# Kernel optimization log

Measured on AMD Instinct MI355X. Metric: run time of the kernel, lower is better.

## Reference

```python
import jax, jax.numpy as jnp
import numpy as np

B, L, D = 2, 1024, 768
NL = 8            # n_layers
DI = 2 * D        # d_inner (expand=2)
NS = 16           # d_state
DR = D // 16      # dt_rank = 48
KC = 4            # d_conv
EPS = 1e-5


def setup_inputs() -> dict:
    key = jax.random.key(0)
    ks = jax.random.split(key, 12)
    s = 0.02
    inp = {
        "x":        jax.random.normal(ks[0], (B, L, D), jnp.float32),
        "ln_w":     jnp.ones((NL, D), jnp.float32),
        "ln_b":     jnp.zeros((NL, D), jnp.float32),
        "in_proj":  jax.random.normal(ks[1], (NL, 2 * DI, D), jnp.float32) * s,
        "conv_w":   jax.random.normal(ks[2], (NL, DI, KC), jnp.float32) * 0.1,
        "conv_b":   jnp.zeros((NL, DI), jnp.float32),
        "x_proj":   jax.random.normal(ks[3], (NL, DR + 2 * NS, DI), jnp.float32) * s,
        "dt_w":     jax.random.normal(ks[4], (NL, DI, DR), jnp.float32) * s,
        "dt_b":     jax.random.normal(ks[5], (NL, DI), jnp.float32) * 0.5,
        "A_log":    jnp.broadcast_to(jnp.log(jnp.arange(1, NS + 1, dtype=jnp.float32)), (NL, DI, NS)).copy(),
        "D_skip":   jnp.ones((NL, DI), jnp.float32),
        "out_proj": jax.random.normal(ks[6], (NL, D, DI), jnp.float32) * s,
        "fn_w":     jnp.ones((D,), jnp.float32),
        "fn_b":     jnp.zeros((D,), jnp.float32),
    }
    return inp


def _layernorm(x, w, b):
    mu = x.mean(-1, keepdims=True)
    var = ((x - mu) ** 2).mean(-1, keepdims=True)
    return (x - mu) * jax.lax.rsqrt(var + EPS) * w + b


def _silu(x):
    return x * jax.nn.sigmoid(x)


def _mamba(xn, Wi, cw, cb, Wx, Wdt, bdt, A_log, Dp, Wo):
    # xn: (B, L, D)
    xz = jnp.einsum('bld,ed->ble', xn, Wi)          # (B, L, 2*DI)
    xi, z = jnp.split(xz, 2, axis=-1)               # each (B, L, DI)
    # causal depthwise conv along L
    xc = jax.lax.conv_general_dilated(
        xi.transpose(0, 2, 1), cw[:, None, :], (1,), [(KC - 1, 0)],
        feature_group_count=DI, dimension_numbers=('NCH', 'OIH', 'NCH'))
    xc = _silu(xc.transpose(0, 2, 1) + cb)          # (B, L, DI)
    dbc = jnp.einsum('ble,re->blr', xc, Wx)         # (B, L, DR+2*NS)
    dt = jax.nn.softplus(jnp.einsum('blr,dr->bld', dbc[..., :DR], Wdt) + bdt)  # (B,L,DI)
    Bm = dbc[..., DR:DR + NS]                        # (B, L, NS)
    Cm = dbc[..., DR + NS:]                          # (B, L, NS)
    A = -jnp.exp(A_log)                              # (DI, NS)

    def step(h, inp):
        dt_t, B_t, C_t, x_t = inp                    # (B,DI),(B,NS),(B,NS),(B,DI)
        dA = jnp.exp(dt_t[..., None] * A)            # (B, DI, NS)
        h = dA * h + (dt_t * x_t)[..., None] * B_t[:, None, :]
        y = jnp.einsum('bdn,bn->bd', h, C_t)
        return h, y

    xs = (dt.transpose(1, 0, 2), Bm.transpose(1, 0, 2),
          Cm.transpose(1, 0, 2), xc.transpose(1, 0, 2))
    h0 = jnp.zeros((xn.shape[0], DI, NS), xn.dtype)
    _, ys = jax.lax.scan(step, h0, xs)               # ys: (L, B, DI)
    y = ys.transpose(1, 0, 2) + xc * Dp
    y = y * _silu(z)
    return jnp.einsum('ble,de->bld', y, Wo)          # (B, L, D)


def reference(x, ln_w, ln_b, in_proj, conv_w, conv_b, x_proj, dt_w, dt_b,
              A_log, D_skip, out_proj, fn_w, fn_b):
    params = (ln_w, ln_b, in_proj, conv_w, conv_b, x_proj, dt_w, dt_b,
              A_log, D_skip, out_proj)

    def block(carry, p):
        xcur, res = carry
        lw, lb, Wi, cw, cb, Wx, Wdt, bdt, Al, Dp, Wo = p
        res = xcur + res                 # residual = x + residual
        xn = _layernorm(xcur, lw, lb)    # norm(x) -- note: norms block input, per source
        h = _mamba(xn, Wi, cw, cb, Wx, Wdt, bdt, Al, Dp, Wo)
        return (h, res), None

    res0 = jnp.zeros_like(x)             # residual=None handled as zeros
    (xf, resf), _ = jax.lax.scan(block, (x, res0), params)
    out = _layernorm(xf + resf, fn_w, fn_b)
    return out
```

## Files before the change

kernel.cpp:

```cpp
#include <hip/hip_runtime.h>
#include <math.h>

#define B_ 2
#define L_ 1024
#define D_ 768
#define NL_ 8
#define DI_ 1536
#define NS_ 16
#define DR_ 48
#define KC_ 4
#define EPS_ 1e-5f
#define M_ (B_*L_)
#define NC_ 64
#define T_ 16
#define KS_ 16
#define KCH_ (DI_/KS_)
#define KDT_ 64

typedef short bf16x8 __attribute__((ext_vector_type(8)));
typedef float f32x4  __attribute__((ext_vector_type(4)));

__device__ __forceinline__ unsigned short f2bf(float f) {
    union { float f; unsigned int u; } v; v.f = f;
    unsigned int u = v.u;
    u += 0x7fffu + ((u >> 16) & 1u);
    return (unsigned short)(u >> 16);
}

__device__ __forceinline__ unsigned int pk2(float a, float b) {
    union { float f; unsigned int u; } va, vb;
    va.f = a; vb.f = b;
    unsigned int ua = va.u + (0x7fffu + ((va.u >> 16) & 1u));
    unsigned int ub = vb.u + (0x7fffu + ((vb.u >> 16) & 1u));
    return (ua >> 16) | (ub & 0xffff0000u);
}

__device__ __forceinline__ void gload16(const void* g, void* l) {
    __builtin_amdgcn_global_load_lds(
        (const __attribute__((address_space(1))) void*)g,
        (__attribute__((address_space(3))) void*)l, 16, 0, 0);
}

__device__ __forceinline__ void cvt_blk(const float* __restrict__ s,
                                        unsigned short* __restrict__ d, int tid) {
    #pragma unroll
    for (int r = 0; r < 4; r++) {
        int off = tid * 4 + r * 1024;
        float4 a = *(const float4*)&s[off];
        uint2 o = {pk2(a.x, a.y), pk2(a.z, a.w)};
        *(uint2*)&d[off] = o;
    }
}

__global__ __launch_bounds__(256) void prep_kernel(
    const float* __restrict__ wi, unsigned short* __restrict__ wi_bf,
    const float* __restrict__ wo, unsigned short* __restrict__ wo_bf,
    const float* __restrict__ wx, unsigned short* __restrict__ wx_bf,
    const float* __restrict__ wdt, unsigned short* __restrict__ wdt_bf,
    const float* __restrict__ A_log, float* __restrict__ negA,
    const float* __restrict__ x, float* __restrict__ xcur,
    float* __restrict__ res,
    unsigned short* __restrict__ dbc_bf) {
    const int E0 = NL_ * 2 * DI_ * D_;
    const int E1 = NL_ * D_ * DI_;
    const int E2 = NL_ * 80 * DI_;
    const int E3 = NL_ * DI_ * KDT_;
    const int E4 = NL_ * DI_ * NS_;
    const int E5 = M_ * D_;
    int tid = threadIdx.x;
    int base = blockIdx.x * 4096;
    if (base < E0) { cvt_blk(wi + base, wi_bf + base, tid); return; }
    base -= E0;
    if (base < E1) { cvt_blk(wo + base, wo_bf + base, tid); return; }
    base -= E1;
    if (base < E2) { cvt_blk(wx + base, wx_bf + base, tid); return; }
    base -= E2;
    if (base < E3) {
        #pragma unroll
        for (int r = 0; r < 4; r++) {
            int off = base + tid * 4 + r * 1024;
            int col = off & (KDT_ - 1);
            uint2 o = {0u, 0u};
            if (col < DR_) {
                float4 a = *(const float4*)&wdt[(size_t)(off >> 6) * DR_ + col];
                o = (uint2){pk2(a.x, a.y), pk2(a.z, a.w)};
            }
            *(uint2*)&wdt_bf[off] = o;
        }
        return;
    }
    base -= E3;
    if (base < E4) {
        #pragma unroll
        for (int r = 0; r < 4; r++) {
            int off = base + tid * 4 + r * 1024;
            float4 a = *(const float4*)&A_log[off];
            float4 o = make_float4(-__expf(a.x), -__expf(a.y),
                                   -__expf(a.z), -__expf(a.w));
            *(float4*)&negA[off] = o;
        }
        return;
    }
    base -= E4;
    if (base < E5) {
        float4 z = make_float4(0.f, 0.f, 0.f, 0.f);
        #pragma unroll
        for (int r = 0; r < 4; r++) {
            int off = base + tid * 4 + r * 1024;
            *(float4*)&xcur[off] = *(const float4*)&x[off];
            *(float4*)&res[off] = z;
        }
        return;
    }
    base -= E5;
    {
        #pragma unroll
        for (int r = 0; r < 4; r++) {
            int off = base + tid * 4 + r * 1024;
            *(uint2*)&dbc_bf[off] = (uint2){0u, 0u};
        }
    }
}

__device__ __forceinline__ float block_sum256(float v) {
    __shared__ float sb[4];
    #pragma unroll
    for (int o = 32; o > 0; o >>= 1) v += __shfl_down(v, o);
    if ((threadIdx.x & 63) == 0) sb[threadIdx.x >> 6] = v;
    __syncthreads();
    float r = sb[0] + sb[1] + sb[2] + sb[3];
    __syncthreads();
    return r;
}

__global__ __launch_bounds__(256) void ln_res_kernel(
    const float* __restrict__ xcur, float* __restrict__ res,
    const float* __restrict__ w, const float* __restrict__ b,
    unsigned short* __restrict__ xn) {
    int row = blockIdx.x;
    int t = threadIdx.x;
    size_t base = (size_t)row * D_;
    float v0 = xcur[base + t];
    float v1 = xcur[base + t + 256];
    float v2 = xcur[base + t + 512];
    res[base + t]       += v0;
    res[base + t + 256] += v1;
    res[base + t + 512] += v2;
    float mu = block_sum256(v0 + v1 + v2) * (1.0f / D_);
    float d0 = v0 - mu, d1 = v1 - mu, d2 = v2 - mu;
    float var = block_sum256(d0 * d0 + d1 * d1 + d2 * d2) * (1.0f / D_);
    float rs = rsqrtf(var + EPS_);
    xn[base + t]       = f2bf(d0 * rs * w[t]       + b[t]);
    xn[base + t + 256] = f2bf(d1 * rs * w[t + 256] + b[t + 256]);
    xn[base + t + 512] = f2bf(d2 * rs * w[t + 512] + b[t + 512]);
}

__global__ __launch_bounds__(256) void final_ln_kernel(
    const float* __restrict__ xcur, const float* __restrict__ res,
    const float* __restrict__ w, const float* __restrict__ b,
    float* __restrict__ out) {
    int row = blockIdx.x;
    int t = threadIdx.x;
    size_t base = (size_t)row * D_;
    float v0 = xcur[base + t]       + res[base + t];
    float v1 = xcur[base + t + 256] + res[base + t + 256];
    float v2 = xcur[base + t + 512] + res[base + t + 512];
    float mu = block_sum256(v0 + v1 + v2) * (1.0f / D_);
    float d0 = v0 - mu, d1 = v1 - mu, d2 = v2 - mu;
    float var = block_sum256(d0 * d0 + d1 * d1 + d2 * d2) * (1.0f / D_);
    float rs = rsqrtf(var + EPS_);
    out[base + t]       = d0 * rs * w[t]       + b[t];
    out[base + t + 256] = d1 * rs * w[t + 256] + b[t + 256];
    out[base + t + 512] = d2 * rs * w[t + 512] + b[t + 512];
}

template <int BM, int BN>
__global__ __launch_bounds__(256) void gemm_bf16_t(
    const unsigned short* __restrict__ A,
    const unsigned short* __restrict__ W,
    float* __restrict__ C, int M, int N, int K) {
    constexpr int FM = BM / 32;
    constexpr int FN = BN / 32;
    constexpr int NLD = (BM + BN) / 64;
    __shared__ unsigned short sA[BM * 32];
    __shared__ unsigned short sW[BN * 32];
    int bm = blockIdx.y * BM, bn = blockIdx.x * BN;
    int tid = threadIdx.x;
    int wave = tid >> 6, lane = tid & 63;
    int wrow = (wave & 1) * (BM / 2), wcol = (wave >> 1) * (BN / 2);
    int quad = lane >> 4, r16 = lane & 15;
    f32x4 acc[FM][FN];
    #pragma unroll
    for (int i = 0; i < FM; i++)
        #pragma unroll
        for (int j = 0; j < FN; j++)
            acc[i][j] = (f32x4){0.f, 0.f, 0.f, 0.f};

    for (int k0 = 0; k0 < K; k0 += 32) {
        #pragma unroll
        for (int r = 0; r < NLD; r++) {
            if (r < BM / 64) {
                int j = r * 256 + tid;
                gload16(&A[(size_t)(bm + (j >> 2)) * K + k0 + (j & 3) * 8],
                        &sA[(r * 256 + wave * 64) * 8]);
            } else {
                int j = (r - BM / 64) * 256 + tid;
                gload16(&W[(size_t)(bn + (j >> 2)) * K + k0 + (j & 3) * 8],
                        &sW[((r - BM / 64) * 256 + wave * 64) * 8]);
            }
        }
        __syncthreads();
        bf16x8 af[FM], wf[FN];
        #pragma unroll
        for (int i = 0; i < FM; i++)
            af[i] = *(const bf16x8*)&sA[(wrow + i * 16 + r16) * 32 + quad * 8];
        #pragma unroll
        for (int j = 0; j < FN; j++)
            wf[j] = *(const bf16x8*)&sW[(wcol + j * 16 + r16) * 32 + quad * 8];
        #pragma unroll
        for (int i = 0; i < FM; i++)
            #pragma unroll
            for (int j = 0; j < FN; j++)
                acc[i][j] = __builtin_amdgcn_mfma_f32_16x16x32_bf16(
                    af[i], wf[j], acc[i][j], 0, 0, 0);
        __syncthreads();
    }
    #pragma unroll
    for (int i = 0; i < FM; i++) {
        #pragma unroll
        for (int j = 0; j < FN; j++) {
            int col = bn + wcol + j * 16 + r16;
            #pragma unroll
            for (int reg = 0; reg < 4; reg++) {
                int row = bm + wrow + i * 16 + quad * 4 + reg;
                C[(size_t)row * N + col] = acc[i][j][reg];
            }
        }
    }
}

__global__ __launch_bounds__(256) void dt_gemm_bf16(
    const unsigned short* __restrict__ A,
    const unsigned short* __restrict__ W,
    const float* __restrict__ bias,
    float* __restrict__ dtb) {
    __shared__ unsigned short sA[128 * 32];
    __shared__ unsigned short sW[128 * 32];
    int bm = blockIdx.y * 128, bn = blockIdx.x * 128;
    int tid = threadIdx.x;
    int wave = tid >> 6, lane = tid & 63;
    int wrow = (wave & 1) * 64, wcol = (wave >> 1) * 64;
    int quad = lane >> 4, r16 = lane & 15;
    f32x4 acc[4][4];
    #pragma unroll
    for (int i = 0; i < 4; i++)
        #pragma unroll
        for (int j = 0; j < 4; j++)
            acc[i][j] = (f32x4){0.f, 0.f, 0.f, 0.f};

    #pragma unroll
    for (int k0 = 0; k0 < KDT_; k0 += 32) {
        #pragma unroll
        for (int r = 0; r < 4; r++) {
            if (r < 2) {
                int j = r * 256 + tid;
                gload16(&A[(size_t)(bm + (j >> 2)) * KDT_ + k0 + (j & 3) * 8],
                        &sA[(r * 256 + wave * 64) * 8]);
            } else {
                int j = (r - 2) * 256 + tid;
                gload16(&W[(size_t)(bn + (j >> 2)) * KDT_ + k0 + (j & 3) * 8],
                        &sW[((r - 2) * 256 + wave * 64) * 8]);
            }
        }
        __syncthreads();
        bf16x8 af[4], wf[4];
        #pragma unroll
        for (int i = 0; i < 4; i++)
            af[i] = *(const bf16x8*)&sA[(wrow + i * 16 + r16) * 32 + quad * 8];
        #pragma unroll
        for (int j = 0; j < 4; j++)
            wf[j] = *(const bf16x8*)&sW[(wcol + j * 16 + r16) * 32 + quad * 8];
        #pragma unroll
        for (int i = 0; i < 4; i++)
            #pragma unroll
            for (int j = 0; j < 4; j++)
                acc[i][j] = __builtin_amdgcn_mfma_f32_16x16x32_bf16(
                    af[i], wf[j], acc[i][j], 0, 0, 0);
        __syncthreads();
    }
    #pragma unroll
    for (int i = 0; i < 4; i++) {
        #pragma unroll
        for (int j = 0; j < 4; j++) {
            int col = bn + wcol + j * 16 + r16;
            float bv = bias[col];
            #pragma unroll
            for (int reg = 0; reg < 4; reg++) {
                int row = bm + wrow + i * 16 + quad * 4 + reg;
                float v = acc[i][j][reg] + bv;
                v = (v > 20.f) ? v : log1pf(__expf(v));
                dtb[(size_t)row * DI_ + col] = v;
            }
        }
    }
}

__global__ __launch_bounds__(256) void conv_xproj_kernel(
    const float* __restrict__ xz,
    const float* __restrict__ cw,
    const float* __restrict__ cb,
    const unsigned short* __restrict__ W,
    float* __restrict__ xcf,
    float* __restrict__ Pb) {
    __shared__ float sxz[67 * 96];
    __shared__ unsigned short sxcb[64 * 104];
    __shared__ float scw[96 * 4];
    __shared__ float scb[96];
    unsigned short* sW = (unsigned short*)sxz;

    int ks = blockIdx.x;
    int bm = blockIdx.y * 64;
    int tid = threadIdx.x;
    int b = bm >> 10, t0 = bm & (L_ - 1);
    int dbase = ks * KCH_;

    if (tid < 96) {
        int d = dbase + tid;
        *(float4*)&scw[tid * 4] = *(const float4*)&cw[d * 4];
        scb[tid] = cb[d];
    }
    for (int j = tid; j < 67 * 24; j += 256) {
        int r = j / 24, c4 = (j % 24) * 4;
        int tt = t0 + r - 3;
        float4 v = make_float4(0.f, 0.f, 0.f, 0.f);
        if (tt >= 0)
            v = *(const float4*)&xz[((size_t)(b * L_ + tt)) * (2 * DI_) + dbase + c4];
        *(float4*)&sxz[r * 96 + c4] = v;
    }
    __syncthreads();
    for (int j = tid; j < 64 * 96; j += 256) {
        int r = j / 96, c = j % 96;
        float acc = scb[c];
        #pragma unroll
        for (int k = 0; k < KC_; k++)
            acc = fmaf(scw[c * 4 + k], sxz[(r + k) * 96 + c], acc);
        float v = acc / (1.0f + __expf(-acc));
        xcf[(size_t)(bm + r) * DI_ + dbase + c] = v;
        sxcb[r * 104 + c] = f2bf(v);
    }
    __syncthreads();
    for (int j = tid; j < 80 * 12; j += 256) {
        int row = j / 12, c16 = (j % 12) * 8;
        *(uint4*)&sW[row * 104 + c16] =
            *(const uint4*)&W[(size_t)row * DI_ + dbase + c16];
    }
    __syncthreads();
    int wave = tid >> 6, lane = tid & 63;
    int quad = lane >> 4, r16 = lane & 15;
    f32x4 acc[5];
    #pragma unroll
    for (int j = 0; j < 5; j++) acc[j] = (f32x4){0.f, 0.f, 0.f, 0.f};
    #pragma unroll
    for (int kk = 0; kk < 3; kk++) {
        bf16x8 af = *(const bf16x8*)&sxcb[(wave * 16 + r16) * 104 + kk * 32 + quad * 8];
        #pragma unroll
        for (int j = 0; j < 5; j++) {
            bf16x8 wf = *(const bf16x8*)&sW[(j * 16 + r16) * 104 + kk * 32 + quad * 8];
            acc[j] = __builtin_amdgcn_mfma_f32_16x16x32_bf16(af, wf, acc[j], 0, 0, 0);
        }
    }
    #pragma unroll
    for (int j = 0; j < 5; j++) {
        int col = j * 16 + r16;
        #pragma unroll
        for (int reg = 0; reg < 4; reg++) {
            int row = bm + wave * 16 + quad * 4 + reg;
            Pb[((size_t)ks * M_ + row) * 80 + col] = acc[j][reg];
        }
    }
}

__global__ void xproj_reduce_kernel(const float* __restrict__ Pb,
                                    unsigned short* __restrict__ dbc_bf,
                                    float* __restrict__ bcp) {
    int i = blockIdx.x * 256 + threadIdx.x;
    float s = 0.f;
    #pragma unroll
    for (int ks = 0; ks < KS_; ks++) s += Pb[(size_t)ks * (M_ * 80) + i];
    int m = i / 80, col = i % 80;
    if (col < DR_) {
        dbc_bf[m * KDT_ + col] = f2bf(s);
    } else if (col < DR_ + NS_) {
        bcp[m * 32 + 2 * (col - DR_)] = s;
    } else {
        bcp[m * 32 + 2 * (col - DR_ - NS_) + 1] = s;
    }
}

__global__ __launch_bounds__(256) void scan_ps_kernel(
    const float* __restrict__ dtb,
    const float* __restrict__ xcf,
    const float4* __restrict__ bcp4,
    const float* __restrict__ negA,
    float* __restrict__ Sb,
    float* __restrict__ sdb) {
    const int NDB = DI_ / 256;
    int bx = blockIdx.x;
    int dblk = bx % NDB;
    int c = (bx / NDB) % NC_;
    int b = bx / (NDB * NC_);
    int d = dblk * 256 + threadIdx.x;

    float A[NS_];
    #pragma unroll
    for (int n = 0; n < NS_; n++) A[n] = negA[(size_t)d * NS_ + n];
    float h[NS_];
    #pragma unroll
    for (int n = 0; n < NS_; n++) h[n] = 0.f;
    float sd = 0.f;

    size_t btbase = (size_t)(b * L_ + c * T_);
    const float* pdt = dtb + btbase * DI_ + d;
    const float* pxc = xcf + btbase * DI_ + d;
    const float4* pbc = bcp4 + btbase * 8;

    #pragma unroll
    for (int t = 0; t < T_; t++) {
        float dt = pdt[(size_t)t * DI_];
        float u  = dt * pxc[(size_t)t * DI_];
        sd += dt;
        #pragma unroll
        for (int q = 0; q < 8; q++) {
            float4 v = pbc[t * 8 + q];
            float e0 = __expf(dt * A[2 * q]);
            h[2 * q] = fmaf(e0, h[2 * q], u * v.x);
            float e1 = __expf(dt * A[2 * q + 1]);
            h[2 * q + 1] = fmaf(e1, h[2 * q + 1], u * v.z);
        }
    }

    size_t o = (((size_t)b * NC_ + c) * DI_ + d) * NS_;
    #pragma unroll
    for (int n = 0; n < NS_; n++) Sb[o + n] = h[n];
    sdb[((size_t)b * NC_ + c) * DI_ + d] = sd;
}

__global__ __launch_bounds__(256) void scan_combine_kernel(
    const float* __restrict__ Sb, const float* __restrict__ sdb,
    const float* __restrict__ negA, float* __restrict__ hin) {
    int i = blockIdx.x * 256 + threadIdx.x;
    int b = i / (DI_ * NS_);
    int rem = i % (DI_ * NS_);
    int d = rem >> 4;
    float Aa = negA[rem];
    const size_t str = (size_t)DI_ * NS_;
    size_t o = (size_t)b * NC_ * str + rem;
    size_t osd = (size_t)b * NC_ * DI_ + d;
    float h = 0.f;
    float s = Sb[o], sd = sdb[osd];
    #pragma unroll 4
    for (int c = 0; c < NC_ - 1; c++) {
        float sn = Sb[o + str];
        float sdn = sdb[osd + DI_];
        hin[o] = h;
        h = fmaf(__expf(Aa * sd), h, s);
        s = sn; sd = sdn;
        o += str; osd += DI_;
    }
    hin[o] = h;
}

__global__ __launch_bounds__(256) void scan_out_kernel(
    const float* __restrict__ dtb, const float* __restrict__ xcf,
    const float4* __restrict__ bcp4, const float* __restrict__ negA,
    const float* __restrict__ hin, const float* __restrict__ xz,
    const float* __restrict__ Dp, unsigned short* __restrict__ yg) {
    const int NDB = DI_ / 256;
    int bx = blockIdx.x;
    int dblk = bx % NDB;
    int c = (bx / NDB) % NC_;
    int b = bx / (NDB * NC_);
    int d = dblk * 256 + threadIdx.x;

    float A[NS_];
    #pragma unroll
    for (int n = 0; n < NS_; n++) A[n] = negA[(size_t)d * NS_ + n];
    size_t o = (((size_t)b * NC_ + c) * DI_ + d) * NS_;
    float h[NS_];
    #pragma unroll
    for (int n = 0; n < NS_; n++) h[n] = hin[o + n];
    float dpv = Dp[d];

    size_t btbase = (size_t)(b * L_ + c * T_);
    const float* pdt = dtb + btbase * DI_ + d;
    const float* pxc = xcf + btbase * DI_ + d;
    const float4* pbc = bcp4 + btbase * 8;

    #pragma unroll
    for (int t = 0; t < T_; t++) {
        float dt = pdt[(size_t)t * DI_];
        float xc = pxc[(size_t)t * DI_];
        float u = dt * xc;
        float y = 0.f;
        #pragma unroll
        for (int q = 0; q < 8; q++) {
            float4 v = pbc[t * 8 + q];
            float e0 = __expf(dt * A[2 * q]);
            h[2 * q] = fmaf(e0, h[2 * q], u * v.x);
            y = fmaf(v.y, h[2 * q], y);
            float e1 = __expf(dt * A[2 * q + 1]);
            h[2 * q + 1] = fmaf(e1, h[2 * q + 1], u * v.z);
            y = fmaf(v.w, h[2 * q + 1], y);
        }
        size_t row = btbase + t;
        float zv = xz[row * (2 * DI_) + DI_ + d];
        float yy = y + xc * dpv;
        yy *= zv / (1.0f + __expf(-zv));
        yg[row * DI_ + d] = f2bf(yy);
    }
}

extern "C" void kernel_launch(void* const* d_in, const int* in_sizes, int n_in,
                              void* d_out, int out_size, void* d_ws, size_t ws_size,
                              hipStream_t stream) {
    const float* x        = (const float*)d_in[0];
    const float* ln_w     = (const float*)d_in[1];
    const float* ln_b     = (const float*)d_in[2];
    const float* in_proj  = (const float*)d_in[3];
    const float* conv_w   = (const float*)d_in[4];
    const float* conv_b   = (const float*)d_in[5];
    const float* x_proj   = (const float*)d_in[6];
    const float* dt_w     = (const float*)d_in[7];
    const float* dt_b     = (const float*)d_in[8];
    const float* A_log    = (const float*)d_in[9];
    const float* D_skip   = (const float*)d_in[10];
    const float* out_proj = (const float*)d_in[11];
    const float* fn_w     = (const float*)d_in[12];
    const float* fn_b     = (const float*)d_in[13];
    float* out = (float*)d_out;

    char* p = (char*)d_ws;
    auto alloc = [&](size_t bytes) {
        char* r = p;
        p += (bytes + 255) & ~(size_t)255;
        return (void*)r;
    };
    float* xcur = (float*)alloc((size_t)M_ * D_ * 4);
    float* res  = (float*)alloc((size_t)M_ * D_ * 4);
    unsigned short* xn = (unsigned short*)alloc((size_t)M_ * D_ * 2);
    float* xz   = (float*)alloc((size_t)M_ * 2 * DI_ * 4);
    float* dtb  = (float*)alloc((size_t)M_ * DI_ * 4);
    float* xcf  = (float*)alloc((size_t)M_ * DI_ * 4);
    unsigned short* dbc_bf = (unsigned short*)alloc((size_t)M_ * KDT_ * 2);
    float* bcp  = (float*)alloc((size_t)M_ * 32 * 4);
    unsigned short* yg = (unsigned short*)alloc((size_t)M_ * DI_ * 2);
    float* Sb   = (float*)alloc((size_t)B_ * NC_ * DI_ * NS_ * 4);
    float* sdb  = (float*)alloc((size_t)B_ * NC_ * DI_ * 4);
    float* hin  = (float*)alloc((size_t)B_ * NC_ * DI_ * NS_ * 4);
    float* Pb   = (float*)alloc((size_t)KS_ * M_ * 80 * 4);
    float* negA = (float*)alloc((size_t)NL_ * DI_ * NS_ * 4);
    const size_t n_wi = (size_t)NL_ * 2 * DI_ * D_;
    const size_t n_wo = (size_t)NL_ * D_ * DI_;
    const size_t n_wx = (size_t)NL_ * 80 * DI_;
    const size_t n_wdt = (size_t)NL_ * DI_ * KDT_;
    unsigned short* wi_bf = (unsigned short*)alloc(n_wi * 2);
    unsigned short* wo_bf = (unsigned short*)alloc(n_wo * 2);
    unsigned short* wx_bf = (unsigned short*)alloc(n_wx * 2);
    unsigned short* wdt_bf = (unsigned short*)alloc(n_wdt * 2);

    prep_kernel<<<7808, 256, 0, stream>>>(
        in_proj, wi_bf, out_proj, wo_bf, x_proj, wx_bf,
        dt_w, wdt_bf, A_log, negA, x, xcur, res, dbc_bf);

    for (int l = 0; l < NL_; l++) {
        const float* negA_l = negA + (size_t)l * DI_ * NS_;

        ln_res_kernel<<<M_, 256, 0, stream>>>(
            xcur, res, ln_w + l * D_, ln_b + l * D_, xn);

        gemm_bf16_t<128, 128><<<dim3((2 * DI_) / 128, M_ / 128), 256, 0, stream>>>(
            xn, wi_bf + (size_t)l * 2 * DI_ * D_, xz, M_, 2 * DI_, D_);

        conv_xproj_kernel<<<dim3(KS_, M_ / 64), 256, 0, stream>>>(
            xz, conv_w + l * DI_ * KC_, conv_b + l * DI_,
            wx_bf + (size_t)l * 80 * DI_, xcf, Pb);
        xproj_reduce_kernel<<<(M_ * 80) / 256, 256, 0, stream>>>(Pb, dbc_bf, bcp);

        dt_gemm_bf16<<<dim3(DI_ / 128, M_ / 128), 256, 0, stream>>>(
            dbc_bf, wdt_bf + (size_t)l * DI_ * KDT_, dt_b + l * DI_, dtb);

        scan_ps_kernel<<<B_ * NC_ * (DI_ / 256), 256, 0, stream>>>(
            dtb, xcf, (const float4*)bcp, negA_l, Sb, sdb);
        scan_combine_kernel<<<(B_ * DI_ * NS_) / 256, 256, 0, stream>>>(
            Sb, sdb, negA_l, hin);
        scan_out_kernel<<<B_ * NC_ * (DI_ / 256), 256, 0, stream>>>(
            dtb, xcf, (const float4*)bcp, negA_l, hin, xz,
            D_skip + (size_t)l * DI_, yg);

        gemm_bf16_t<128, 64><<<dim3(D_ / 64, M_ / 128), 256, 0, stream>>>(
            yg, wo_bf + (size_t)l * D_ * DI_, xcur, M_, D_, DI_);
    }

    final_ln_kernel<<<M_, 256, 0, stream>>>(xcur, res, fn_w, fn_b, out);
}
```

Before: 1.408 ms.

## Use one wave per row in layernorms, vectorize prep, retune scan combine

```diff
diff --git a/kernel.cpp b/kernel.cpp
--- a/kernel.cpp
+++ b/kernel.cpp
@@ -43,13 +43,15 @@
 
 __device__ __forceinline__ void cvt_blk(const float* __restrict__ s,
                                         unsigned short* __restrict__ d, int tid) {
-    #pragma unroll
-    for (int r = 0; r < 4; r++) {
-        int off = tid * 4 + r * 1024;
-        float4 a = *(const float4*)&s[off];
-        uint2 o = {pk2(a.x, a.y), pk2(a.z, a.w)};
-        *(uint2*)&d[off] = o;
-    }
+    int o = tid * 4;
+    float4 a0 = *(const float4*)&s[o];
+    float4 a1 = *(const float4*)&s[o + 1024];
+    float4 a2 = *(const float4*)&s[o + 2048];
+    float4 a3 = *(const float4*)&s[o + 3072];
+    *(uint2*)&d[o]        = (uint2){pk2(a0.x, a0.y), pk2(a0.z, a0.w)};
+    *(uint2*)&d[o + 1024] = (uint2){pk2(a1.x, a1.y), pk2(a1.z, a1.w)};
+    *(uint2*)&d[o + 2048] = (uint2){pk2(a2.x, a2.y), pk2(a2.z, a2.w)};
+    *(uint2*)&d[o + 3072] = (uint2){pk2(a3.x, a3.y), pk2(a3.z, a3.w)};
 }
 
 __global__ __launch_bounds__(256) void prep_kernel(
@@ -76,102 +78,161 @@
     if (base < E2) { cvt_blk(wx + base, wx_bf + base, tid); return; }
     base -= E2;
     if (base < E3) {
-        #pragma unroll
-        for (int r = 0; r < 4; r++) {
-            int off = base + tid * 4 + r * 1024;
-            int col = off & (KDT_ - 1);
-            uint2 o = {0u, 0u};
-            if (col < DR_) {
-                float4 a = *(const float4*)&wdt[(size_t)(off >> 6) * DR_ + col];
-                o = (uint2){pk2(a.x, a.y), pk2(a.z, a.w)};
-            }
-            *(uint2*)&wdt_bf[off] = o;
+        int off0 = base + tid * 4;
+        int col = off0 & (KDT_ - 1);
+        if (col < DR_) {
+            float4 a0 = *(const float4*)&wdt[(size_t)((off0) >> 6) * DR_ + col];
+            float4 a1 = *(const float4*)&wdt[(size_t)((off0 + 1024) >> 6) * DR_ + col];
+            float4 a2 = *(const float4*)&wdt[(size_t)((off0 + 2048) >> 6) * DR_ + col];
+            float4 a3 = *(const float4*)&wdt[(size_t)((off0 + 3072) >> 6) * DR_ + col];
+            *(uint2*)&wdt_bf[off0]        = (uint2){pk2(a0.x, a0.y), pk2(a0.z, a0.w)};
+            *(uint2*)&wdt_bf[off0 + 1024] = (uint2){pk2(a1.x, a1.y), pk2(a1.z, a1.w)};
+            *(uint2*)&wdt_bf[off0 + 2048] = (uint2){pk2(a2.x, a2.y), pk2(a2.z, a2.w)};
+            *(uint2*)&wdt_bf[off0 + 3072] = (uint2){pk2(a3.x, a3.y), pk2(a3.z, a3.w)};
+        } else {
+            uint2 z = {0u, 0u};
+            *(uint2*)&wdt_bf[off0] = z;
+            *(uint2*)&wdt_bf[off0 + 1024] = z;
+            *(uint2*)&wdt_bf[off0 + 2048] = z;
+            *(uint2*)&wdt_bf[off0 + 3072] = z;
         }
         return;
     }
     base -= E3;
     if (base < E4) {
-        #pragma unroll
-        for (int r = 0; r < 4; r++) {
-            int off = base + tid * 4 + r * 1024;
-            float4 a = *(const float4*)&A_log[off];
-            float4 o = make_float4(-__expf(a.x), -__expf(a.y),
-                                   -__expf(a.z), -__expf(a.w));
-            *(float4*)&negA[off] = o;
-        }
+        int off0 = base + tid * 4;
+        float4 a0 = *(const float4*)&A_log[off0];
+        float4 a1 = *(const float4*)&A_log[off0 + 1024];
+        float4 a2 = *(const float4*)&A_log[off0 + 2048];
+        float4 a3 = *(const float4*)&A_log[off0 + 3072];
+        *(float4*)&negA[off0] = make_float4(-__expf(a0.x), -__expf(a0.y), -__expf(a0.z), -__expf(a0.w));
+        *(float4*)&negA[off0 + 1024] = make_float4(-__expf(a1.x), -__expf(a1.y), -__expf(a1.z), -__expf(a1.w));
+        *(float4*)&negA[off0 + 2048] = make_float4(-__expf(a2.x), -__expf(a2.y), -__expf(a2.z), -__expf(a2.w));
+        *(float4*)&negA[off0 + 3072] = make_float4(-__expf(a3.x), -__expf(a3.y), -__expf(a3.z), -__expf(a3.w));
         return;
     }
     base -= E4;
     if (base < E5) {
+        int off0 = base + tid * 4;
+        float4 a0 = *(const float4*)&x[off0];
+        float4 a1 = *(const float4*)&x[off0 + 1024];
+        float4 a2 = *(const float4*)&x[off0 + 2048];
+        float4 a3 = *(const float4*)&x[off0 + 3072];
         float4 z = make_float4(0.f, 0.f, 0.f, 0.f);
-        #pragma unroll
-        for (int r = 0; r < 4; r++) {
-            int off = base + tid * 4 + r * 1024;
-            *(float4*)&xcur[off] = *(const float4*)&x[off];
-            *(float4*)&res[off] = z;
-        }
+        *(float4*)&xcur[off0] = a0;        *(float4*)&res[off0] = z;
+        *(float4*)&xcur[off0 + 1024] = a1; *(float4*)&res[off0 + 1024] = z;
+        *(float4*)&xcur[off0 + 2048] = a2; *(float4*)&res[off0 + 2048] = z;
+        *(float4*)&xcur[off0 + 3072] = a3; *(float4*)&res[off0 + 3072] = z;
         return;
     }
     base -= E5;
     {
-        #pragma unroll
-        for (int r = 0; r < 4; r++) {
-            int off = base + tid * 4 + r * 1024;
-            *(uint2*)&dbc_bf[off] = (uint2){0u, 0u};
-        }
-    }
-}
-
-__device__ __forceinline__ float block_sum256(float v) {
-    __shared__ float sb[4];
+        int off0 = base + tid * 4;
+        uint2 z = {0u, 0u};
+        *(uint2*)&dbc_bf[off0] = z;
+        *(uint2*)&dbc_bf[off0 + 1024] = z;
+        *(uint2*)&dbc_bf[off0 + 2048] = z;
+        *(uint2*)&dbc_bf[off0 + 3072] = z;
+    }
+}
+
+__device__ __forceinline__ float wave_sum(float v) {
     #pragma unroll
     for (int o = 32; o > 0; o >>= 1) v += __shfl_down(v, o);
-    if ((threadIdx.x & 63) == 0) sb[threadIdx.x >> 6] = v;
-    __syncthreads();
-    float r = sb[0] + sb[1] + sb[2] + sb[3];
-    __syncthreads();
-    return r;
+    return __shfl(v, 0);
 }
 
 __global__ __launch_bounds__(256) void ln_res_kernel(
     const float* __restrict__ xcur, float* __restrict__ res,
     const float* __restrict__ w, const float* __restrict__ b,
     unsigned short* __restrict__ xn) {
-    int row = blockIdx.x;
-    int t = threadIdx.x;
+    int wave = threadIdx.x >> 6, lane = threadIdx.x & 63;
+    int row = blockIdx.x * 4 + wave;
     size_t base = (size_t)row * D_;
-    float v0 = xcur[base + t];
-    float v1 = xcur[base + t + 256];
-    float v2 = xcur[base + t + 512];
-    res[base + t]       += v0;
-    res[base + t + 256] += v1;
-    res[base + t + 512] += v2;
-    float mu = block_sum256(v0 + v1 + v2) * (1.0f / D_);
-    float d0 = v0 - mu, d1 = v1 - mu, d2 = v2 - mu;
-    float var = block_sum256(d0 * d0 + d1 * d1 + d2 * d2) * (1.0f / D_);
+    int off = lane * 4;
+    float4 v0 = *(const float4*)&xcur[base + off];
+    float4 v1 = *(const float4*)&xcur[base + off + 256];
+    float4 v2 = *(const float4*)&xcur[base + off + 512];
+    float4 r0 = *(const float4*)&res[base + off];
+    float4 r1 = *(const float4*)&res[base + off + 256];
+    float4 r2 = *(const float4*)&res[base + off + 512];
+    r0.x += v0.x; r0.y += v0.y; r0.z += v0.z; r0.w += v0.w;
+    r1.x += v1.x; r1.y += v1.y; r1.z += v1.z; r1.w += v1.w;
+    r2.x += v2.x; r2.y += v2.y; r2.z += v2.z; r2.w += v2.w;
+    *(float4*)&res[base + off]       = r0;
+    *(float4*)&res[base + off + 256] = r1;
+    *(float4*)&res[base + off + 512] = r2;
+    float s = (v0.x + v0.y + v0.z + v0.w) + (v1.x + v1.y + v1.z + v1.w)
+            + (v2.x + v2.y + v2.z + v2.w);
+    float mu = wave_sum(s) * (1.0f / D_);
+    float4 d0 = make_float4(v0.x - mu, v0.y - mu, v0.z - mu, v0.w - mu);
+    float4 d1 = make_float4(v1.x - mu, v1.y - mu, v1.z - mu, v1.w - mu);
+    float4 d2 = make_float4(v2.x - mu, v2.y - mu, v2.z - mu, v2.w - mu);
+    float sv = d0.x * d0.x + d0.y * d0.y + d0.z * d0.z + d0.w * d0.w
+             + d1.x * d1.x + d1.y * d1.y + d1.z * d1.z + d1.w * d1.w
+             + d2.x * d2.x + d2.y * d2.y + d2.z * d2.z + d2.w * d2.w;
+    float var = wave_sum(sv) * (1.0f / D_);
     float rs = rsqrtf(var + EPS_);
-    xn[base + t]       = f2bf(d0 * rs * w[t]       + b[t]);
-    xn[base + t + 256] = f2bf(d1 * rs * w[t + 256] + b[t + 256]);
-    xn[base + t + 512] = f2bf(d2 * rs * w[t + 512] + b[t + 512]);
+    float4 w0 = *(const float4*)&w[off];
+    float4 w1 = *(const float4*)&w[off + 256];
+    float4 w2 = *(const float4*)&w[off + 512];
+    float4 b0 = *(const float4*)&b[off];
+    float4 b1 = *(const float4*)&b[off + 256];
+    float4 b2 = *(const float4*)&b[off + 512];
+    *(uint2*)&xn[base + off] = (uint2){
+        pk2(d0.x * rs * w0.x + b0.x, d0.y * rs * w0.y + b0.y),
+        pk2(d0.z * rs * w0.z + b0.z, d0.w * rs * w0.w + b0.w)};
+    *(uint2*)&xn[base + off + 256] = (uint2){
+        pk2(d1.x * rs * w1.x + b1.x, d1.y * rs * w1.y + b1.y),
+        pk2(d1.z * rs * w1.z + b1.z, d1.w * rs * w1.w + b1.w)};
+    *(uint2*)&xn[base + off + 512] = (uint2){
+        pk2(d2.x * rs * w2.x + b2.x, d2.y * rs * w2.y + b2.y),
+        pk2(d2.z * rs * w2.z + b2.z, d2.w * rs * w2.w + b2.w)};
 }
 
 __global__ __launch_bounds__(256) void final_ln_kernel(
     const float* __restrict__ xcur, const float* __restrict__ res,
     const float* __restrict__ w, const float* __restrict__ b,
     float* __restrict__ out) {
-    int row = blockIdx.x;
-    int t = threadIdx.x;
+    int wave = threadIdx.x >> 6, lane = threadIdx.x & 63;
+    int row = blockIdx.x * 4 + wave;
     size_t base = (size_t)row * D_;
-    float v0 = xcur[base + t]       + res[base + t];
-    float v1 = xcur[base + t + 256] + res[base + t + 256];
-    float v2 = xcur[base + t + 512] + res[base + t + 512];
-    float mu = block_sum256(v0 + v1 + v2) * (1.0f / D_);
-    float d0 = v0 - mu, d1 = v1 - mu, d2 = v2 - mu;
-    float var = block_sum256(d0 * d0 + d1 * d1 + d2 * d2) * (1.0f / D_);
+    int off = lane * 4;
+    float4 v0 = *(const float4*)&xcur[base + off];
+    float4 v1 = *(const float4*)&xcur[base + off + 256];
+    float4 v2 = *(const float4*)&xcur[base + off + 512];
+    float4 r0 = *(const float4*)&res[base + off];
+    float4 r1 = *(const float4*)&res[base + off + 256];
+    float4 r2 = *(const float4*)&res[base + off + 512];
+    v0.x += r0.x; v0.y += r0.y; v0.z += r0.z; v0.w += r0.w;
+    v1.x += r1.x; v1.y += r1.y; v1.z += r1.z; v1.w += r1.w;
+    v2.x += r2.x; v2.y += r2.y; v2.z += r2.z; v2.w += r2.w;
+    float s = (v0.x + v0.y + v0.z + v0.w) + (v1.x + v1.y + v1.z + v1.w)
+            + (v2.x + v2.y + v2.z + v2.w);
+    float mu = wave_sum(s) * (1.0f / D_);
+    float4 d0 = make_float4(v0.x - mu, v0.y - mu, v0.z - mu, v0.w - mu);
+    float4 d1 = make_float4(v1.x - mu, v1.y - mu, v1.z - mu, v1.w - mu);
+    float4 d2 = make_float4(v2.x - mu, v2.y - mu, v2.z - mu, v2.w - mu);
+    float sv = d0.x * d0.x + d0.y * d0.y + d0.z * d0.z + d0.w * d0.w
+             + d1.x * d1.x + d1.y * d1.y + d1.z * d1.z + d1.w * d1.w
+             + d2.x * d2.x + d2.y * d2.y + d2.z * d2.z + d2.w * d2.w;
+    float var = wave_sum(sv) * (1.0f / D_);
     float rs = rsqrtf(var + EPS_);
-    out[base + t]       = d0 * rs * w[t]       + b[t];
-    out[base + t + 256] = d1 * rs * w[t + 256] + b[t + 256];
-    out[base + t + 512] = d2 * rs * w[t + 512] + b[t + 512];
+    float4 w0 = *(const float4*)&w[off];
+    float4 w1 = *(const float4*)&w[off + 256];
+    float4 w2 = *(const float4*)&w[off + 512];
+    float4 b0 = *(const float4*)&b[off];
+    float4 b1 = *(const float4*)&b[off + 256];
+    float4 b2 = *(const float4*)&b[off + 512];
+    *(float4*)&out[base + off] = make_float4(
+        d0.x * rs * w0.x + b0.x, d0.y * rs * w0.y + b0.y,
+        d0.z * rs * w0.z + b0.z, d0.w * rs * w0.w + b0.w);
+    *(float4*)&out[base + off + 256] = make_float4(
+        d1.x * rs * w1.x + b1.x, d1.y * rs * w1.y + b1.y,
+        d1.z * rs * w1.z + b1.z, d1.w * rs * w1.w + b1.w);
+    *(float4*)&out[base + off + 512] = make_float4(
+        d2.x * rs * w2.x + b2.x, d2.y * rs * w2.y + b2.y,
+        d2.z * rs * w2.z + b2.z, d2.w * rs * w2.w + b2.w);
 }
 
 template <int BM, int BN>
@@ -445,10 +506,10 @@
     sdb[((size_t)b * NC_ + c) * DI_ + d] = sd;
 }
 
-__global__ __launch_bounds__(256) void scan_combine_kernel(
+__global__ __launch_bounds__(64) void scan_combine_kernel(
     const float* __restrict__ Sb, const float* __restrict__ sdb,
     const float* __restrict__ negA, float* __restrict__ hin) {
-    int i = blockIdx.x * 256 + threadIdx.x;
+    int i = blockIdx.x * 64 + threadIdx.x;
     int b = i / (DI_ * NS_);
     int rem = i % (DI_ * NS_);
     int d = rem >> 4;
@@ -457,17 +518,27 @@
     size_t o = (size_t)b * NC_ * str + rem;
     size_t osd = (size_t)b * NC_ * DI_ + d;
     float h = 0.f;
-    float s = Sb[o], sd = sdb[osd];
-    #pragma unroll 4
-    for (int c = 0; c < NC_ - 1; c++) {
-        float sn = Sb[o + str];
-        float sdn = sdb[osd + DI_];
-        hin[o] = h;
-        h = fmaf(__expf(Aa * sd), h, s);
-        s = sn; sd = sdn;
-        o += str; osd += DI_;
-    }
-    hin[o] = h;
+    float s0 = Sb[o],           sd0 = sdb[osd];
+    float s1 = Sb[o + str],     sd1 = sdb[osd + DI_];
+    float s2 = Sb[o + 2 * str], sd2 = sdb[osd + 2 * DI_];
+    float s3 = Sb[o + 3 * str], sd3 = sdb[osd + 3 * DI_];
+    for (int c = 0; c < NC_ - 4; c += 4) {
+        float n0 = Sb[o + 4 * str], nd0 = sdb[osd + 4 * DI_];
+        float n1 = Sb[o + 5 * str], nd1 = sdb[osd + 5 * DI_];
+        float n2 = Sb[o + 6 * str], nd2 = sdb[osd + 6 * DI_];
+        float n3 = Sb[o + 7 * str], nd3 = sdb[osd + 7 * DI_];
+        hin[o] = h;           h = fmaf(__expf(Aa * sd0), h, s0);
+        hin[o + str] = h;     h = fmaf(__expf(Aa * sd1), h, s1);
+        hin[o + 2 * str] = h; h = fmaf(__expf(Aa * sd2), h, s2);
+        hin[o + 3 * str] = h; h = fmaf(__expf(Aa * sd3), h, s3);
+        s0 = n0; sd0 = nd0; s1 = n1; sd1 = nd1;
+        s2 = n2; sd2 = nd2; s3 = n3; sd3 = nd3;
+        o += 4 * str; osd += 4 * DI_;
+    }
+    hin[o] = h;           h = fmaf(__expf(Aa * sd0), h, s0);
+    hin[o + str] = h;     h = fmaf(__expf(Aa * sd1), h, s1);
+    hin[o + 2 * str] = h; h = fmaf(__expf(Aa * sd2), h, s2);
+    hin[o + 3 * str] = h;
 }
 
 __global__ __launch_bounds__(256) void scan_out_kernel(
@@ -575,7 +646,7 @@
     for (int l = 0; l < NL_; l++) {
         const float* negA_l = negA + (size_t)l * DI_ * NS_;
 
-        ln_res_kernel<<<M_, 256, 0, stream>>>(
+        ln_res_kernel<<<M_ / 4, 256, 0, stream>>>(
             xcur, res, ln_w + l * D_, ln_b + l * D_, xn);
 
         gemm_bf16_t<128, 128><<<dim3((2 * DI_) / 128, M_ / 128), 256, 0, stream>>>(
@@ -591,7 +662,7 @@
 
         scan_ps_kernel<<<B_ * NC_ * (DI_ / 256), 256, 0, stream>>>(
             dtb, xcf, (const float4*)bcp, negA_l, Sb, sdb);
-        scan_combine_kernel<<<(B_ * DI_ * NS_) / 256, 256, 0, stream>>>(
+        scan_combine_kernel<<<(B_ * DI_ * NS_) / 64, 64, 0, stream>>>(
             Sb, sdb, negA_l, hin);
         scan_out_kernel<<<B_ * NC_ * (DI_ / 256), 256, 0, stream>>>(
             dtb, xcf, (const float4*)bcp, negA_l, hin, xz,
@@ -601,5 +672,5 @@
             yg, wo_bf + (size_t)l * D_ * DI_, xcur, M_, D_, DI_);
     }
 
-    final_ln_kernel<<<M_, 256, 0, stream>>>(xcur, res, fn_w, fn_b, out);
-}
+    final_ln_kernel<<<M_ / 4, 256, 0, stream>>>(xcur, res, fn_w, fn_b, out);
+}
```

After: 1.350 ms. 4.1% less time.
